# Optimization experiments

Hardware: AMD Instinct MI355X
Metric: run time of the kernel (lower is better)

Reference implementation:

```python
import jax, jax.numpy as jnp
import numpy as np

RCUT = 6.0      # cutoff radius
AXIS = 16       # axis_neuron
NORM = 64.0     # normalizer = avg_neighbors + 1 (precomputed stat)
EPS = 1e-15
NTYPES = 2


def _embed(h, W0, b0, W1, b1, W2, b2):
    # tiny per-type-pair embedding MLP: scalar sr -> C channels
    h = jnp.tanh(h @ W0 + b0)
    h = jnp.tanh(h @ W1 + b1)
    return jnp.tanh(h @ W2 + b2)


def _forward(coord_3N, box_33, srmean, srstd, xrsrstd, Gbias, Ebias,
             emb_W0, emb_b0, emb_W1, emb_b1, emb_W2, emb_b2,
             fit_W0, fit_b0, fit_W1, fit_b1, fit_W2, fit_b2, n1):
    N = coord_3N.shape[1]
    L = jnp.diagonal(box_33)  # orthorhombic box lengths (3,)
    # relative coords with minimum-image convention: x[d,i,j] = c[d,j] - c[d,i]
    x_3NM = coord_3N[:, None, :] - coord_3N[:, :, None]
    x_3NM = x_3NM - L[:, None, None] * jnp.round(x_3NM / L[:, None, None])
    eye = jnp.eye(N, dtype=bool)
    r_NM = jnp.sqrt(jnp.where(eye, 1.0, (x_3NM ** 2).sum(0)))  # diag masked for safe grad
    # smooth switching / r  (DeepPot-SE style sr)
    u = r_NM / RCUT
    sw = jnp.where((r_NM < RCUT) & (~eye), ((-6.0 * u + 15.0) * u - 10.0) * u ** 3 + 1.0, 0.0)
    sr_NM = sw / r_NM
    rsr_NM = sr_NM / r_NM
    idx = (0, n1, N)  # contiguous type boundaries (atoms sorted by type)
    rows_sr, rows_rsr, rows_emb = [], [], []
    for i in range(NTYPES):
        sr_i = sr_NM[idx[i]:idx[i + 1]]
        rows_sr.append(sr_i / srstd[i])
        rows_rsr.append(rsr_NM[idx[i]:idx[i + 1]] / xrsrstd[i])
        srn_i = (sr_i - srmean[i]) / srstd[i]
        blocks = []
        for j in range(NTYPES):
            p = NTYPES * i + j  # type-pair index
            blocks.append(_embed(srn_i[:, idx[j]:idx[j + 1], None],
                                 emb_W0[p], emb_b0[p], emb_W1[p], emb_b1[p], emb_W2[p], emb_b2[p]))
        rows_emb.append(jnp.concatenate(blocks, axis=1))
    srbias_NM = jnp.concatenate(rows_sr, axis=0)
    R_3NM = (jnp.concatenate(rows_rsr, axis=0)[None] + EPS) * x_3NM  # e3norm = 1
    embed_NMC = jnp.concatenate(rows_emb, axis=0)
    # weighted reductions over neighbor axis M (einsum avoids the 3*N*M*C temp)
    Ginv_NC = jnp.einsum('nm,nmc->nc', srbias_NM, embed_NMC) / NORM
    Geqv_3NC = jnp.einsum('dnm,nmc->dnc', R_3NM, embed_NMC) / NORM
    G_4NC = jnp.concatenate([(Ginv_NC + Gbias)[None], Geqv_3NC], axis=0)
    # equivariant outer-product descriptor: Feat[n,a,c] = sum_k G[k,n,c]*G[k,n,a]
    Feat_NX = jnp.einsum('knc,kna->nac', G_4NC, G_4NC[:, :, :AXIS]).reshape(N, -1)
    energy = jnp.zeros((), dtype=Feat_NX.dtype)
    for i in range(NTYPES):
        h = Feat_NX[idx[i]:idx[i + 1]]
        h = jnp.tanh(h @ fit_W0[i] + fit_b0[i])
        h = jnp.tanh(h @ fit_W1[i] + fit_b1[i])
        h = h @ fit_W2[i] + fit_b2[i]
        energy = energy + (h + Ebias[i]).sum()
    return energy


def setup_inputs() -> dict:
    key = jax.random.key(0)
    ks = jax.random.split(key, 20)
    N, N1, BOXL = 1024, 512, 20.0
    W = (16, 32, 64)
    X, F = AXIS * W[-1], 128

    def wt(k, shape, fan_in):
        return jax.random.normal(k, shape, jnp.float32) / np.float32(np.sqrt(fan_in))

    return {
        'coord_3N': jax.random.uniform(ks[0], (3, N), jnp.float32) * BOXL,
        'box_33': BOXL * jnp.eye(3, dtype=jnp.float32),
        'srmean': 0.1 * jax.random.uniform(ks[1], (NTYPES,), jnp.float32),
        'srstd': 0.5 + jax.random.uniform(ks[2], (NTYPES,), jnp.float32),
        'xrsrstd': 0.5 + jax.random.uniform(ks[3], (NTYPES,), jnp.float32),
        'Gbias': 0.1 * jax.random.normal(ks[4], (W[2],), jnp.float32),
        'Ebias': jax.random.normal(ks[5], (NTYPES,), jnp.float32),
        'emb_W0': wt(ks[6], (4, 1, W[0]), 1),
        'emb_b0': 0.1 * jax.random.normal(ks[7], (4, W[0]), jnp.float32),
        'emb_W1': wt(ks[8], (4, W[0], W[1]), W[0]),
        'emb_b1': 0.1 * jax.random.normal(ks[9], (4, W[1]), jnp.float32),
        'emb_W2': wt(ks[10], (4, W[1], W[2]), W[1]),
        'emb_b2': 0.1 * jax.random.normal(ks[11], (4, W[2]), jnp.float32),
        'fit_W0': wt(ks[12], (NTYPES, X, F), X),
        'fit_b0': 0.1 * jax.random.normal(ks[13], (NTYPES, F), jnp.float32),
        'fit_W1': wt(ks[14], (NTYPES, F, F), F),
        'fit_b1': 0.1 * jax.random.normal(ks[15], (NTYPES, F), jnp.float32),
        'fit_W2': wt(ks[16], (NTYPES, F, 1), F),
        'fit_b2': 0.1 * jax.random.normal(ks[17], (NTYPES, 1), jnp.float32),
        'n1': N1,
    }


def reference(coord_3N, box_33, srmean, srstd, xrsrstd, Gbias, Ebias,
              emb_W0, emb_b0, emb_W1, emb_b1, emb_W2, emb_b2,
              fit_W0, fit_b0, fit_W1, fit_b1, fit_W2, fit_b2, n1):
    return _forward(coord_3N, box_33, srmean, srstd, xrsrstd, Gbias, Ebias,
                    emb_W0, emb_b0, emb_W1, emb_b1, emb_W2, emb_b2,
                    fit_W0, fit_b0, fit_W1, fit_b1, fit_W2, fit_b2, n1)
```

## Files before the change

### kernel.cpp

```cpp
#include <hip/hip_runtime.h>

#define RCUT 6.0f

typedef _Float16 h2v __attribute__((ext_vector_type(2)));
typedef _Float16 h8  __attribute__((ext_vector_type(8)));
typedef float    f4  __attribute__((ext_vector_type(4)));

__device__ __forceinline__ float fast_tanh(float x) {
    float e = __expf(2.0f * x);
    return 1.0f - 2.0f * __builtin_amdgcn_rcpf(e + 1.0f);
}

__device__ __forceinline__ h2v pkh(float a, float b) {
#if __has_builtin(__builtin_amdgcn_cvt_pkrtz)
    union { __fp16 __attribute__((ext_vector_type(2))) r; h2v h; } u;
    u.r = __builtin_amdgcn_cvt_pkrtz(a, b);
    return u.h;
#else
    h2v r; r.x = (_Float16)a; r.y = (_Float16)b; return r;
#endif
}

__global__ __launch_bounds__(256, 2) void k_embed(
    const float* __restrict__ coord, const float* __restrict__ box,
    const float* __restrict__ srmean, const float* __restrict__ srstd,
    const float* __restrict__ xrsrstd, const float* __restrict__ Gbias,
    const float* __restrict__ eW0, const float* __restrict__ eb0,
    const float* __restrict__ eW1, const float* __restrict__ eb1,
    const float* __restrict__ eW2, const float* __restrict__ eb2,
    const int* __restrict__ n1p,
    const float* __restrict__ fW0, const float* __restrict__ fW1,
    h2v* __restrict__ feat, _Float16* __restrict__ W0ht,
    _Float16* __restrict__ W1ht, unsigned int* __restrict__ counter, int N)
{
    const int nb  = blockIdx.x;
    const int tid = threadIdx.x;
    const int NB  = N >> 1;

    __shared__ float s_w0[2][16], s_b0[2][16];
    __shared__ __align__(16) _Float16 s_srn[1024];
    __shared__ __align__(16) _Float16 s_cf[4][1024];
    __shared__ __align__(16) _Float16 s_h1[128][32];
    __shared__ __align__(16) _Float16 s_ef[4][4][64][8];
    __shared__ unsigned short s_nbr[1024];
    __shared__ float s_g4[2][256];
    __shared__ __align__(16) _Float16 w1t[2][32][24];
    __shared__ __align__(16) _Float16 w2t[2][64][40];
    __shared__ int s_wA[4], s_wB[4];

    if (nb >= NB) {
        const int b = nb - NB;
        if (b == 0 && tid == 0) *counter = 0u;
        float (*s_t)[33] = reinterpret_cast<float(*)[33]>(&s_ef[0][0][0][0]);
        if (b < 256) {
            int type = b >> 7, tb = b & 127;
            int ki = tb >> 2, ci = tb & 3;
            const float* src = fW0 + (size_t)type * 131072;
            int c = tid & 31, r0 = (tid >> 5) * 4;
            #pragma unroll
            for (int q = 0; q < 4; q++)
                s_t[r0 + q][c] = src[(size_t)(ki * 32 + r0 + q) * 128 + ci * 32 + c];
            __syncthreads();
            _Float16* dst = W0ht + (size_t)type * 131072;
            int kk = tid & 31, c0 = (tid >> 5) * 4;
            #pragma unroll
            for (int q = 0; q < 4; q++)
                dst[(size_t)(ci * 32 + c0 + q) * 1024 + ki * 32 + kk] = (_Float16)s_t[kk][c0 + q];
        } else {
            int b2v = b - 256, type = b2v >> 4, tb = b2v & 15;
            int ki = tb >> 2, ci = tb & 3;
            const float* src = fW1 + (size_t)type * 16384;
            int c = tid & 31, r0 = (tid >> 5) * 4;
            #pragma unroll
            for (int q = 0; q < 4; q++)
                s_t[r0 + q][c] = src[(size_t)(ki * 32 + r0 + q) * 128 + ci * 32 + c];
            __syncthreads();
            _Float16* dst = W1ht + (size_t)type * 16384;
            int kk = tid & 31, c0 = (tid >> 5) * 4;
            #pragma unroll
            for (int q = 0; q < 4; q++)
                dst[(size_t)(ci * 32 + c0 + q) * 128 + ki * 32 + kk] = (_Float16)s_t[kk][c0 + q];
        }
        return;
    }

    const int nA = 2 * nb, nBt = 2 * nb + 1;
    const int n1 = *n1p;
    const int ti = (nA >= n1) ? 1 : 0;
    const int wid = tid >> 6, lane = tid & 63;
    const int l15 = lane & 15, lk = lane >> 4;

    for (int t = tid; t < 32; t += 256) { int j = t >> 4, f = t & 15;
        s_w0[j][f] = eW0[(2 * ti + j) * 16 + f];
        s_b0[j][f] = eb0[(2 * ti + j) * 16 + f]; }
    for (int idx = tid; idx < 1024; idx += 256) {
        int j = idx >> 9, r = idx & 511, f = r >> 5, g = r & 31;
        w1t[j][g][f] = (_Float16)eW1[(2 * ti + j) * 512 + f * 32 + g];
    }
    for (int idx = tid; idx < 4096; idx += 256) {
        int j = idx >> 11, r = idx & 2047, g = r >> 6, c = r & 63;
        w2t[j][c][g] = (_Float16)eW2[(2 * ti + j) * 2048 + g * 64 + c];
    }
    float b1r[2][2], b2r[2][4];
    #pragma unroll
    for (int j = 0; j < 2; j++) {
        #pragma unroll
        for (int q = 0; q < 2; q++) b1r[j][q] = eb1[(2 * ti + j) * 32 + 16 * q + l15];
        #pragma unroll
        for (int q = 0; q < 4; q++) b2r[j][q] = eb2[(2 * ti + j) * 64 + 16 * q + l15];
    }

    const float Lx = box[0], Ly = box[4], Lz = box[8];
    const float iLx = 1.0f / Lx, iLy = 1.0f / Ly, iLz = 1.0f / Lz;
    const float xA = coord[nA], yA = coord[N + nA], zA = coord[2 * N + nA];
    const float xB = coord[nBt], yB = coord[N + nBt], zB = coord[2 * N + nBt];
    const float srm  = srmean[ti];
    const float isrs = 1.0f / srstd[ti];
    const float ixrs = 1.0f / xrsrstd[ti];

    unsigned long long balA[4], balB[4];
    {
        int wA = 0, wB = 0;
        const int mystart = wid * 256;
        #pragma unroll
        for (int r = 0; r < 4; r++) {
            int m = mystart + r * 64 + lane;
            float x = coord[m], y = coord[N + m], z = coord[2 * N + m];
            float ax = x - xA; ax -= Lx * rintf(ax * iLx);
            float ay = y - yA; ay -= Ly * rintf(ay * iLy);
            float az = z - zA; az -= Lz * rintf(az * iLz);
            float ra = ax * ax + ay * ay + az * az;
            float bx = x - xB; bx -= Lx * rintf(bx * iLx);
            float by = y - yB; by -= Ly * rintf(by * iLy);
            float bz = z - zB; bz -= Lz * rintf(bz * iLz);
            float rb = bx * bx + by * by + bz * bz;
            bool pA = (ra < RCUT * RCUT) && (m != nA);
            bool pB = (rb < RCUT * RCUT) && (m != nBt);
            balA[r] = __ballot(pA);
            balB[r] = __ballot(pB);
            wA += (int)__popcll(balA[r]);
            wB += (int)__popcll(balB[r]);
        }
        if (lane == 0) { s_wA[wid] = wA; s_wB[wid] = wB; }
    }
    __syncthreads();
    int cntA = s_wA[0] + s_wA[1] + s_wA[2] + s_wA[3];
    int cntB = s_wB[0] + s_wB[1] + s_wB[2] + s_wB[3];
    int cnt  = cntA + cntB;
    if (cnt > 1024) cnt = 1024;
    if (cntA > 1024) cntA = 1024;
    {
        int baseA = 0, baseB = cntA;
        for (int w = 0; w < wid; w++) { baseA += s_wA[w]; baseB += s_wB[w]; }
        const unsigned long long lt = (1ull << lane) - 1ull;
        const int mystart = wid * 256;
        #pragma unroll
        for (int r = 0; r < 4; r++) {
            int m = mystart + r * 64 + lane;
            float x = coord[m], y = coord[N + m], z = coord[2 * N + m];
            #pragma unroll
            for (int cc = 0; cc < 2; cc++) {
                unsigned long long bal = cc ? balB[r] : balA[r];
                int base = cc ? baseB : baseA;
                if ((bal >> lane) & 1ull) {
                    int pos = base + (int)__popcll(bal & lt);
                    if (pos < 1024) {
                        float dx = x - (cc ? xB : xA); dx -= Lx * rintf(dx * iLx);
                        float dy = y - (cc ? yB : yA); dy -= Ly * rintf(dy * iLy);
                        float dz = z - (cc ? zB : zA); dz -= Lz * rintf(dz * iLz);
                        float r2 = dx * dx + dy * dy + dz * dz;
                        float rr = sqrtf(r2);
                        float rinv = __builtin_amdgcn_rcpf(rr);
                        float u  = rr * (1.0f / RCUT);
                        float u3 = u * u * u;
                        float sw_ = ((-6.0f * u + 15.0f) * u - 10.0f) * u3 + 1.0f;
                        float sr  = sw_ * rinv;
                        float crs = sr * rinv * ixrs + 1e-15f;
                        s_srn[pos]   = (_Float16)((sr - srm) * isrs);
                        s_cf[0][pos] = (_Float16)(sr * isrs);
                        s_cf[1][pos] = (_Float16)(crs * dx);
                        s_cf[2][pos] = (_Float16)(crs * dy);
                        s_cf[3][pos] = (_Float16)(crs * dz);
                        s_nbr[pos]   = (unsigned short)m;
                    }
                }
                if (cc) baseB += (int)__popcll(bal);
                else    baseA += (int)__popcll(bal);
            }
        }
    }
    __syncthreads();
    const int ntiles = (cnt + 127) >> 7;
    for (int i = cnt + tid; i < ntiles * 128; i += 256) {
        s_srn[i] = (_Float16)0.0f; s_nbr[i] = 0;
        s_cf[0][i] = (_Float16)0.0f; s_cf[1][i] = (_Float16)0.0f;
        s_cf[2][i] = (_Float16)0.0f; s_cf[3][i] = (_Float16)0.0f;
    }
    __syncthreads();

    f4 gacc = {0.0f, 0.0f, 0.0f, 0.0f};
    const f4 zf4 = {0.0f, 0.0f, 0.0f, 0.0f};

    for (int t = 0; t < ntiles; t++) {
        const int t128 = t << 7;
        __syncthreads();

        #pragma unroll
        for (int mt2 = 0; mt2 < 2; mt2++) {
            const int mt = 2 * wid + mt2;
            const int row = 16 * mt + l15;
            const int rp = t128 + row;
            float srn = (float)s_srn[rp];
            int jr = (s_nbr[rp] >= n1) ? 1 : 0;
            h8 a = {};
            if (lk < 2) {
                const float* wp = &s_w0[jr][8 * lk];
                const float* bp = &s_b0[jr][8 * lk];
                #pragma unroll
                for (int q = 0; q < 8; q++)
                    a[q] = (_Float16)fast_tanh(fmaf(srn, wp[q], bp[q]));
            }
            #pragma unroll
            for (int nt1 = 0; nt1 < 2; nt1++) {
                const int c = 16 * nt1 + l15;
                h8 b0f = {}, b1f = {};
                if (lk < 2) {
                    b0f = *(const h8*)&w1t[0][c][8 * lk];
                    b1f = *(const h8*)&w1t[1][c][8 * lk];
                }
                f4 d0 = __builtin_amdgcn_mfma_f32_16x16x32_f16(a, b0f, zf4, 0, 0, 0);
                f4 d1 = __builtin_amdgcn_mfma_f32_16x16x32_f16(a, b1f, zf4, 0, 0, 0);
                #pragma unroll
                for (int r = 0; r < 4; r++) {
                    int gp = 16 * mt + 4 * lk + r;
                    bool is0 = (s_nbr[t128 + gp] < n1);
                    float hv = fast_tanh((is0 ? d0[r] : d1[r]) + (is0 ? b1r[0][nt1] : b1r[1][nt1]));
                    int e = 16 * nt1 + l15;
                    s_h1[gp][(((e >> 3) ^ ((gp >> 1) & 3)) << 3) + (e & 7)] = (_Float16)hv;
                }
            }
        }
        asm volatile("" ::: "memory");
        #pragma unroll
        for (int mt2 = 0; mt2 < 2; mt2++) {
            const int mt = 2 * wid + mt2;
            const int row = 16 * mt + l15;
            h8 a2 = *(const h8*)&s_h1[row][((lk ^ ((row >> 1) & 3)) << 3)];
            #pragma unroll
            for (int nt = 0; nt < 4; nt++) {
                const int c = 16 * nt + l15;
                h8 w20 = *(const h8*)&w2t[0][c][8 * lk];
                h8 w21 = *(const h8*)&w2t[1][c][8 * lk];
                f4 e0 = __builtin_amdgcn_mfma_f32_16x16x32_f16(a2, w20, zf4, 0, 0, 0);
                f4 e1 = __builtin_amdgcn_mfma_f32_16x16x32_f16(a2, w21, zf4, 0, 0, 0);
                #pragma unroll
                for (int r = 0; r < 4; r++) {
                    int gp = 16 * mt + 4 * lk + r;
                    bool is0 = (s_nbr[t128 + gp] < n1);
                    float ev = fast_tanh((is0 ? e0[r] : e1[r]) + (is0 ? b2r[0][nt] : b2r[1][nt]));
                    s_ef[nt][gp >> 5][l15 + 16 * ((gp & 31) >> 3)][gp & 7] = (_Float16)ev;
                }
            }
        }
        __syncthreads();

        #pragma unroll
        for (int ks = 0; ks < 4; ks++) {
            const int s = t128 + 32 * ks;
            h8 ac = {};
            if (l15 < 8) {
                const bool rowA = l15 < 4;
                const int  cr   = rowA ? l15 : (l15 - 4);
                const bool allA = (s + 31) < cntA;
                const bool allB = s >= cntA;
                if ((allA && rowA) || (allB && !rowA)) {
                    ac = *(const h8*)&s_cf[cr][s + 8 * lk];
                } else if (!allA && !allB) {
                    #pragma unroll
                    for (int r = 0; r < 8; r++) {
                        int p = s + 8 * lk + r;
                        bool isA = p < cntA;
                        if (isA == rowA) ac[r] = s_cf[cr][p];
                    }
                }
            }
            h8 eb = *(const h8*)&s_ef[wid][ks][lane][0];
            gacc = __builtin_amdgcn_mfma_f32_16x16x32_f16(ac, eb, gacc, 0, 0, 0);
        }
    }

    if (lk < 2) {
        float* sg = &s_g4[lk][0];
        #pragma unroll
        for (int r = 0; r < 4; r++) {
            float gv = gacc[r] * (1.0f / 64.0f);
            if (r == 0) gv += Gbias[16 * wid + l15];
            sg[r * 64 + 16 * wid + l15] = gv;
        }
    }
    __syncthreads();
    #pragma unroll
    for (int at = 0; at < 2; at++) {
        const float* sg = &s_g4[at][0];
        h2v* outp = feat + (size_t)(2 * nb + at) * 512;
        #pragma unroll
        for (int q = 0; q < 2; q++) {
            int o2 = tid + 256 * q;
            int a = o2 >> 5, c = (2 * o2) & 63;
            float ga0 = sg[a],       ga1 = sg[64 + a];
            float ga2 = sg[128 + a], ga3 = sg[192 + a];
            float s0 = ga0 * sg[c];
            s0 = fmaf(ga1, sg[64 + c],  s0);
            s0 = fmaf(ga2, sg[128 + c], s0);
            s0 = fmaf(ga3, sg[192 + c], s0);
            float s1 = ga0 * sg[c + 1];
            s1 = fmaf(ga1, sg[64 + c + 1],  s1);
            s1 = fmaf(ga2, sg[128 + c + 1], s1);
            s1 = fmaf(ga3, sg[192 + c + 1], s1);
            outp[o2] = pkh(s0, s1);
        }
    }
}

__global__ __launch_bounds__(512) void k_fit(
    const _Float16* __restrict__ featf, const _Float16* __restrict__ W0ht,
    const _Float16* __restrict__ W1ht,
    const float* __restrict__ b0, const float* __restrict__ b1,
    const float* __restrict__ W2, const float* __restrict__ b2,
    const float* __restrict__ Ebias, const int* __restrict__ n1p,
    unsigned int* __restrict__ counter, float* __restrict__ slots,
    float* __restrict__ out)
{
    __shared__ float s_red[4][2][16][64];
    __shared__ __align__(16) _Float16 s_hd[16][128];
    __shared__ float s_sum[16][32];

    const int tid = threadIdx.x;
    const int lane = tid & 63, w = tid >> 6;
    const int kq = w >> 1, ch = w & 1;
    const int l15 = lane & 15, lk = lane >> 4;
    const int n0 = blockIdx.x * 16;
    const int ia = (n0 >= *n1p) ? 1 : 0;
    const f4 zf4 = {0.0f, 0.0f, 0.0f, 0.0f};

    const _Float16* Ap = featf + (size_t)(n0 + l15) * 1024 + kq * 256;
    const _Float16* B0 = W0ht + (size_t)ia * 131072 + kq * 256;
    f4 acc[4] = {zf4, zf4, zf4, zf4};
    #pragma unroll
    for (int ks = 0; ks < 8; ks++) {
        h8 a = *(const h8*)(Ap + ks * 32 + 8 * lk);
        #pragma unroll
        for (int nt = 0; nt < 4; nt++) {
            const int c = ch * 64 + nt * 16 + l15;
            h8 b = *(const h8*)(B0 + (size_t)c * 1024 + ks * 32 + 8 * lk);
            acc[nt] = __builtin_amdgcn_mfma_f32_16x16x32_f16(a, b, acc[nt], 0, 0, 0);
        }
    }
    #pragma unroll
    for (int nt = 0; nt < 4; nt++)
        #pragma unroll
        for (int r = 0; r < 4; r++)
            s_red[kq][ch][4 * lk + r][nt * 16 + l15] = acc[nt][r];
    __syncthreads();

    {
        const int row = tid >> 5, c0 = (tid & 31) * 4;
        const int chh = c0 >> 6, cl = c0 & 63;
        f4 v = *(const f4*)&s_red[0][chh][row][cl];
        v += *(const f4*)&s_red[1][chh][row][cl];
        v += *(const f4*)&s_red[2][chh][row][cl];
        v += *(const f4*)&s_red[3][chh][row][cl];
        #pragma unroll
        for (int q = 0; q < 4; q++) {
            int c = c0 + q;
            float h = fast_tanh(v[q] + b0[ia * 128 + c]);
            s_hd[row][(((c >> 3) ^ row) << 3) + (c & 7)] = (_Float16)h;
        }
    }
    __syncthreads();

    f4 acc1[4] = {zf4, zf4, zf4, zf4};
    {
        h8 a = *(const h8*)&s_hd[l15][(((4 * kq + lk) ^ l15) & 15) << 3];
        const _Float16* B1 = W1ht + (size_t)ia * 16384 + kq * 32;
        #pragma unroll
        for (int nt = 0; nt < 4; nt++) {
            const int c = ch * 64 + nt * 16 + l15;
            h8 b = *(const h8*)(B1 + (size_t)c * 128 + 8 * lk);
            acc1[nt] = __builtin_amdgcn_mfma_f32_16x16x32_f16(a, b, zf4, 0, 0, 0);
        }
    }
    #pragma unroll
    for (int nt = 0; nt < 4; nt++)
        #pragma unroll
        for (int r = 0; r < 4; r++)
            s_red[kq][ch][4 * lk + r][nt * 16 + l15] = acc1[nt][r];
    __syncthreads();

    {
        const int row = tid >> 5, c0 = (tid & 31) * 4;
        const int chh = c0 >> 6, cl = c0 & 63;
        f4 v = *(const f4*)&s_red[0][chh][row][cl];
        v += *(const f4*)&s_red[1][chh][row][cl];
        v += *(const f4*)&s_red[2][chh][row][cl];
        v += *(const f4*)&s_red[3][chh][row][cl];
        float pv = 0.0f;
        #pragma unroll
        for (int q = 0; q < 4; q++) {
            int c = c0 + q;
            pv += fast_tanh(v[q] + b1[ia * 128 + c]) * W2[ia * 128 + c];
        }
        s_sum[row][tid & 31] = pv;
    }
    __syncthreads();
    if (w == 0) {
        const int row = lane >> 2, g = lane & 3;
        float s = 0.0f;
        #pragma unroll
        for (int i = 0; i < 8; i++) s += s_sum[row][8 * g + i];
        s += __shfl_xor(s, 1);  s += __shfl_xor(s, 2);
        s += __shfl_xor(s, 4);  s += __shfl_xor(s, 8);
        s += __shfl_xor(s, 16); s += __shfl_xor(s, 32);
        if (lane == 0) {
            float e = s + 16.0f * (b2[ia] + Ebias[ia]);
            slots[blockIdx.x] = e;
            __threadfence();
            unsigned int old = atomicAdd(counter, 1u);
            if (old == 63u) {
                __threadfence();
                float tot = 0.0f;
                for (int i = 0; i < 64; i++)
                    tot += __hip_atomic_load(&slots[i], __ATOMIC_RELAXED, __HIP_MEMORY_SCOPE_AGENT);
                out[0] = tot;
            }
        }
    }
}

extern "C" void kernel_launch(void* const* d_in, const int* in_sizes, int n_in,
                              void* d_out, int out_size, void* d_ws, size_t ws_size,
                              hipStream_t stream) {
    const float* coord   = (const float*)d_in[0];
    const float* box     = (const float*)d_in[1];
    const float* srmean  = (const float*)d_in[2];
    const float* srstd   = (const float*)d_in[3];
    const float* xrsrstd = (const float*)d_in[4];
    const float* Gbias   = (const float*)d_in[5];
    const float* Ebias   = (const float*)d_in[6];
    const float* eW0     = (const float*)d_in[7];
    const float* eb0     = (const float*)d_in[8];
    const float* eW1     = (const float*)d_in[9];
    const float* eb1     = (const float*)d_in[10];
    const float* eW2     = (const float*)d_in[11];
    const float* eb2     = (const float*)d_in[12];
    const float* fW0     = (const float*)d_in[13];
    const float* fb0     = (const float*)d_in[14];
    const float* fW1     = (const float*)d_in[15];
    const float* fb1     = (const float*)d_in[16];
    const float* fW2     = (const float*)d_in[17];
    const float* fb2     = (const float*)d_in[18];
    const int*   n1p     = (const int*)d_in[19];

    const int N = in_sizes[0] / 3;
    h2v*      featbuf = (h2v*)d_ws;
    _Float16* W0ht = (_Float16*)((char*)d_ws + (size_t)2 * 1024 * 1024);
    _Float16* W1ht = W0ht + 2 * 131072;
    char* tail = (char*)d_ws + (size_t)(2 * 1024 + 512 + 64) * 1024;
    unsigned int* counter = (unsigned int*)tail;
    float*        slots   = (float*)(tail + 64);

    k_embed<<<N / 2 + 288, 256, 0, stream>>>(coord, box, srmean, srstd, xrsrstd,
                                             Gbias, eW0, eb0, eW1, eb1, eW2, eb2,
                                             n1p, fW0, fW1, featbuf, W0ht, W1ht,
                                             counter, N);
    k_fit<<<N / 16, 512, 0, stream>>>((const _Float16*)featbuf, W0ht, W1ht,
                                      fb0, fb1, fW2, fb2, Ebias, n1p,
                                      counter, slots, (float*)d_out);
}
```

Measured before the change: 39.37 us.

## Halve fit-kernel rows per block, move prep blocks first, use rational tanh

Three changes. k_fit now processes 8 atoms per block instead of 16, doubling the grid to 128 blocks so more CUs get work; the upper MFMA rows compute duplicated data that is discarded, and the final reduction counter and slot count become 128. The weight-transpose prep blocks in k_embed move to the front of the grid so they are scheduled first. fast_tanh is replaced by a clamped Padé rational approximation, which avoids the exp but is less accurate for large inputs.

```diff
diff --git a/kernel.cpp b/kernel.cpp
--- a/kernel.cpp
+++ b/kernel.cpp
@@ -1,14 +1,18 @@
 #include <hip/hip_runtime.h>
 
 #define RCUT 6.0f
+#define NPREP 288
 
 typedef _Float16 h2v __attribute__((ext_vector_type(2)));
 typedef _Float16 h8  __attribute__((ext_vector_type(8)));
 typedef float    f4  __attribute__((ext_vector_type(4)));
 
 __device__ __forceinline__ float fast_tanh(float x) {
-    float e = __expf(2.0f * x);
-    return 1.0f - 2.0f * __builtin_amdgcn_rcpf(e + 1.0f);
+    float x2 = x * x;
+    float num = x * fmaf(x2, fmaf(x2, 1.0f, 105.0f), 945.0f);
+    float den = fmaf(x2, fmaf(x2, 15.0f, 420.0f), 945.0f);
+    float r = num * __builtin_amdgcn_rcpf(den);
+    return fminf(fmaxf(r, -1.0f), 1.0f);
 }
 
 __device__ __forceinline__ h2v pkh(float a, float b) {
@@ -33,9 +37,7 @@
     h2v* __restrict__ feat, _Float16* __restrict__ W0ht,
     _Float16* __restrict__ W1ht, unsigned int* __restrict__ counter, int N)
 {
-    const int nb  = blockIdx.x;
     const int tid = threadIdx.x;
-    const int NB  = N >> 1;
 
     __shared__ float s_w0[2][16], s_b0[2][16];
     __shared__ __align__(16) _Float16 s_srn[1024];
@@ -48,8 +50,8 @@
     __shared__ __align__(16) _Float16 w2t[2][64][40];
     __shared__ int s_wA[4], s_wB[4];
 
-    if (nb >= NB) {
-        const int b = nb - NB;
+    if (blockIdx.x < NPREP) {
+        const int b = blockIdx.x;
         if (b == 0 && tid == 0) *counter = 0u;
         float (*s_t)[33] = reinterpret_cast<float(*)[33]>(&s_ef[0][0][0][0]);
         if (b < 256) {
@@ -84,6 +86,7 @@
         return;
     }
 
+    const int nb  = blockIdx.x - NPREP;
     const int nA = 2 * nb, nBt = 2 * nb + 1;
     const int n1 = *n1p;
     const int ti = (nA >= n1) ? 1 : 0;
@@ -331,19 +334,20 @@
     unsigned int* __restrict__ counter, float* __restrict__ slots,
     float* __restrict__ out)
 {
-    __shared__ float s_red[4][2][16][64];
-    __shared__ __align__(16) _Float16 s_hd[16][128];
-    __shared__ float s_sum[16][32];
+    __shared__ float s_red[4][2][8][64];
+    __shared__ __align__(16) _Float16 s_hd[8][128];
+    __shared__ float s_sum[8][32];
 
     const int tid = threadIdx.x;
     const int lane = tid & 63, w = tid >> 6;
     const int kq = w >> 1, ch = w & 1;
     const int l15 = lane & 15, lk = lane >> 4;
-    const int n0 = blockIdx.x * 16;
+    const int row8 = l15 & 7;
+    const int n0 = blockIdx.x * 8;
     const int ia = (n0 >= *n1p) ? 1 : 0;
     const f4 zf4 = {0.0f, 0.0f, 0.0f, 0.0f};
 
-    const _Float16* Ap = featf + (size_t)(n0 + l15) * 1024 + kq * 256;
+    const _Float16* Ap = featf + (size_t)(n0 + row8) * 1024 + kq * 256;
     const _Float16* B0 = W0ht + (size_t)ia * 131072 + kq * 256;
     f4 acc[4] = {zf4, zf4, zf4, zf4};
     #pragma unroll
@@ -356,14 +360,16 @@
             acc[nt] = __builtin_amdgcn_mfma_f32_16x16x32_f16(a, b, acc[nt], 0, 0, 0);
         }
     }
-    #pragma unroll
-    for (int nt = 0; nt < 4; nt++)
-        #pragma unroll
-        for (int r = 0; r < 4; r++)
-            s_red[kq][ch][4 * lk + r][nt * 16 + l15] = acc[nt][r];
-    __syncthreads();
-
-    {
+    if (lk < 2) {
+        #pragma unroll
+        for (int nt = 0; nt < 4; nt++)
+            #pragma unroll
+            for (int r = 0; r < 4; r++)
+                s_red[kq][ch][4 * lk + r][nt * 16 + l15] = acc[nt][r];
+    }
+    __syncthreads();
+
+    if (tid < 256) {
         const int row = tid >> 5, c0 = (tid & 31) * 4;
         const int chh = c0 >> 6, cl = c0 & 63;
         f4 v = *(const f4*)&s_red[0][chh][row][cl];
@@ -374,14 +380,14 @@
         for (int q = 0; q < 4; q++) {
             int c = c0 + q;
             float h = fast_tanh(v[q] + b0[ia * 128 + c]);
-            s_hd[row][(((c >> 3) ^ row) << 3) + (c & 7)] = (_Float16)h;
+            s_hd[row][((((c >> 3) ^ row) & 15) << 3) + (c & 7)] = (_Float16)h;
         }
     }
     __syncthreads();
 
     f4 acc1[4] = {zf4, zf4, zf4, zf4};
     {
-        h8 a = *(const h8*)&s_hd[l15][(((4 * kq + lk) ^ l15) & 15) << 3];
+        h8 a = *(const h8*)&s_hd[row8][(((4 * kq + lk) ^ row8) & 15) << 3];
         const _Float16* B1 = W1ht + (size_t)ia * 16384 + kq * 32;
         #pragma unroll
         for (int nt = 0; nt < 4; nt++) {
@@ -390,14 +396,16 @@
             acc1[nt] = __builtin_amdgcn_mfma_f32_16x16x32_f16(a, b, zf4, 0, 0, 0);
         }
     }
-    #pragma unroll
-    for (int nt = 0; nt < 4; nt++)
-        #pragma unroll
-        for (int r = 0; r < 4; r++)
-            s_red[kq][ch][4 * lk + r][nt * 16 + l15] = acc1[nt][r];
-    __syncthreads();
-
-    {
+    if (lk < 2) {
+        #pragma unroll
+        for (int nt = 0; nt < 4; nt++)
+            #pragma unroll
+            for (int r = 0; r < 4; r++)
+                s_red[kq][ch][4 * lk + r][nt * 16 + l15] = acc1[nt][r];
+    }
+    __syncthreads();
+
+    if (tid < 256) {
         const int row = tid >> 5, c0 = (tid & 31) * 4;
         const int chh = c0 >> 6, cl = c0 & 63;
         f4 v = *(const f4*)&s_red[0][chh][row][cl];
@@ -414,22 +422,23 @@
     }
     __syncthreads();
     if (w == 0) {
-        const int row = lane >> 2, g = lane & 3;
+        const int row = lane >> 3, g = lane & 7;
         float s = 0.0f;
         #pragma unroll
-        for (int i = 0; i < 8; i++) s += s_sum[row][8 * g + i];
+        for (int i = 0; i < 4; i++) s += s_sum[row][4 * g + i];
         s += __shfl_xor(s, 1);  s += __shfl_xor(s, 2);
-        s += __shfl_xor(s, 4);  s += __shfl_xor(s, 8);
-        s += __shfl_xor(s, 16); s += __shfl_xor(s, 32);
+        s += __shfl_xor(s, 4);
+        s += __shfl_xor(s, 8);  s += __shfl_xor(s, 16);
+        s += __shfl_xor(s, 32);
         if (lane == 0) {
-            float e = s + 16.0f * (b2[ia] + Ebias[ia]);
+            float e = s + 8.0f * (b2[ia] + Ebias[ia]);
             slots[blockIdx.x] = e;
             __threadfence();
             unsigned int old = atomicAdd(counter, 1u);
-            if (old == 63u) {
+            if (old == 127u) {
                 __threadfence();
                 float tot = 0.0f;
-                for (int i = 0; i < 64; i++)
+                for (int i = 0; i < 128; i++)
                     tot += __hip_atomic_load(&slots[i], __ATOMIC_RELAXED, __HIP_MEMORY_SCOPE_AGENT);
                 out[0] = tot;
             }
@@ -469,11 +478,11 @@
     unsigned int* counter = (unsigned int*)tail;
     float*        slots   = (float*)(tail + 64);
 
-    k_embed<<<N / 2 + 288, 256, 0, stream>>>(coord, box, srmean, srstd, xrsrstd,
-                                             Gbias, eW0, eb0, eW1, eb1, eW2, eb2,
-                                             n1p, fW0, fW1, featbuf, W0ht, W1ht,
-                                             counter, N);
-    k_fit<<<N / 16, 512, 0, stream>>>((const _Float16*)featbuf, W0ht, W1ht,
-                                      fb0, fb1, fW2, fb2, Ebias, n1p,
-                                      counter, slots, (float*)d_out);
+    k_embed<<<N / 2 + NPREP, 256, 0, stream>>>(coord, box, srmean, srstd, xrsrstd,
+                                               Gbias, eW0, eb0, eW1, eb1, eW2, eb2,
+                                               n1p, fW0, fW1, featbuf, W0ht, W1ht,
+                                               counter, N);
+    k_fit<<<N / 8, 512, 0, stream>>>((const _Float16*)featbuf, W0ht, W1ht,
+                                     fb0, fb1, fW2, fb2, Ebias, n1p,
+                                     counter, slots, (float*)d_out);
 }
```

Result: slower. 46.10 us (+17.1%).
